# Performance work log

Measured on AMD Instinct MI355X. Metric: run time of the kernel, lower is better.

The kernel has to match this reference:

```python
import jax, jax.numpy as jnp
import numpy as np

N_NODES = 100000
N_EDGES = 1600000
IN_CH = 128
OUT_CH = 32
HID = 2 * OUT_CH


def setup_inputs() -> dict:
    key = jax.random.key(0)
    k1, k2, k3, k4 = jax.random.split(key, 4)
    x = jax.random.normal(k1, (N_NODES, IN_CH), dtype=jnp.float32)
    edge_index = jax.random.randint(k2, (2, N_EDGES), 0, N_NODES, dtype=jnp.int64)
    W1 = jax.random.normal(k3, (IN_CH, HID), dtype=jnp.float32) / np.sqrt(IN_CH)
    b1 = jnp.zeros((HID,), dtype=jnp.float32)
    W2 = jax.random.normal(k4, (HID, OUT_CH), dtype=jnp.float32) / np.sqrt(HID)
    b2 = jnp.zeros((OUT_CH,), dtype=jnp.float32)
    return {"x": x, "edge_index": edge_index, "W1": W1, "b1": b1, "W2": W2, "b2": b2}


def _gcn_norm(edge_index, n_nodes):
    # GCNConv default: add self-loops, symmetric deg^{-1/2} normalization.
    loop = jnp.arange(n_nodes, dtype=edge_index.dtype)
    src = jnp.concatenate([edge_index[0], loop])
    dst = jnp.concatenate([edge_index[1], loop])
    deg = jax.ops.segment_sum(jnp.ones_like(dst, dtype=jnp.float32), dst, num_segments=n_nodes)
    dinv = jnp.where(deg > 0, jax.lax.rsqrt(deg), 0.0)
    norm = dinv[src] * dinv[dst]  # [E + N]
    return src, dst, norm


def _gcn_conv(h, W, b, src, dst, norm, n_nodes):
    m = h @ W                      # transform first (small GEMM)
    msg = m[src] * norm[:, None]   # gather + scale per edge
    agg = jax.ops.segment_sum(msg, dst, num_segments=n_nodes)  # scatter-add
    return agg + b


def reference(x, edge_index, W1, b1, W2, b2):
    n = x.shape[0]
    src, dst, norm = _gcn_norm(edge_index, n)
    h = jax.nn.relu(_gcn_conv(x, W1, b1, src, dst, norm, n))
    return _gcn_conv(h, W2, b2, src, dst, norm, n)
```

## Files before the change

kernel.cpp:

```cpp
#include <hip/hip_runtime.h>

#define IN_CH 128
#define HID 64
#define OUT_CH 32
#define BUCKET_CAP 6144
#define NB_MAX 512

typedef _Float16 f16x8 __attribute__((ext_vector_type(8)));
typedef float f32x4 __attribute__((ext_vector_type(4)));

__device__ __forceinline__ unsigned short f32_to_bf16(float f) {
    union { float f; unsigned int u; } v; v.f = f;
    unsigned int u = v.u;
    u += 0x7FFFu + ((u >> 16) & 1u);
    return (unsigned short)(u >> 16);
}
__device__ __forceinline__ float bf16_to_f32(unsigned short h) {
    union { unsigned int u; float f; } v; v.u = ((unsigned int)h) << 16;
    return v.f;
}
__device__ __forceinline__ float bf16_lo(unsigned int u) {
    union { unsigned int u; float f; } v; v.u = u << 16; return v.f;
}
__device__ __forceinline__ float bf16_hi(unsigned int u) {
    union { unsigned int u; float f; } v; v.u = u & 0xFFFF0000u; return v.f;
}

__device__ __forceinline__ int load_idx(const void* e, long long i, int is64) {
    if (is64) return ((const int*)e)[2 * i];
    return ((const int*)e)[i];
}

__global__ __launch_bounds__(256) void binA_kernel(
    const void* __restrict__ edges, long long E,
    int* __restrict__ bucket_cur, unsigned int* __restrict__ entries, int nb) {
    __shared__ int hist[NB_MAX];
    __shared__ int cbase[NB_MAX];
    __shared__ int s_is64;
    const int tid = threadIdx.x;

    if (tid < 64) {
        int v = ((const int*)edges)[2 * tid + 1];
        unsigned long long nz = __ballot(v != 0);
        if (tid == 0) s_is64 = (nz == 0ull) ? 1 : 0;
    }
    for (int i = tid; i < nb; i += 256) hist[i] = 0;
    __syncthreads();
    const int is64 = s_is64;

    const long long per = (E + gridDim.x - 1) / gridDim.x;
    const long long lo = blockIdx.x * per;
    const long long hi = (lo + per < E) ? lo + per : E;

    for (long long i = lo + tid; i < hi; i += 256) {
        int dst = load_idx(edges, E + i, is64);
        atomicAdd(&hist[dst >> 8], 1);
    }
    __syncthreads();
    for (int i = tid; i < nb; i += 256) {
        int c = hist[i];
        int base = (c > 0) ? atomicAdd(&bucket_cur[i], c) : 0;
        cbase[i] = base;
        hist[i] = 0;
    }
    __syncthreads();
    for (long long i = lo + tid; i < hi; i += 256) {
        int src = load_idx(edges, i, is64);
        int dst = load_idx(edges, E + i, is64);
        int b = dst >> 8;
        int rel = cbase[b] + atomicAdd(&hist[b], 1);
        if (rel < BUCKET_CAP)
            entries[(long long)b * BUCKET_CAP + rel] = ((unsigned)src << 8) | (unsigned)(dst & 255);
    }
}

__global__ __launch_bounds__(256) void binB1_kernel(
    const unsigned int* __restrict__ entries, const int* __restrict__ bucket_cur,
    int* __restrict__ counts, int* __restrict__ row_off, float* __restrict__ dinv,
    int n) {
    __shared__ int hist[256];
    __shared__ int scan[256];
    const int b   = blockIdx.x;
    const int tid = threadIdx.x;
    const long long seg = (long long)b * BUCKET_CAP;
    int cnt = bucket_cur[b];
    if (cnt > BUCKET_CAP) cnt = BUCKET_CAP;

    hist[tid] = 0;
    __syncthreads();
    for (int i = tid; i < cnt; i += 256)
        atomicAdd(&hist[entries[seg + i] & 255], 1);
    __syncthreads();

    int v = hist[tid];
    scan[tid] = v;
    __syncthreads();
    for (int off = 1; off < 256; off <<= 1) {
        int t = (tid >= off) ? scan[tid - off] : 0;
        __syncthreads();
        scan[tid] += t;
        __syncthreads();
    }
    int ex = scan[tid] - v;
    int node = (b << 8) + tid;
    if (node < n) {
        counts[node]  = v;
        row_off[node] = (int)seg + ex;
        dinv[node]    = rsqrtf((float)v + 1.0f);
    }
}

__global__ __launch_bounds__(256) void binB2_kernel(
    const unsigned int* __restrict__ entries, const int* __restrict__ bucket_cur,
    const int* __restrict__ row_off, const float* __restrict__ dinv,
    int2* __restrict__ ew, int n) {
    __shared__ int cur[256];
    __shared__ float ldi[256];
    const int b   = blockIdx.x;
    const int tid = threadIdx.x;
    const long long seg = (long long)b * BUCKET_CAP;
    int cnt = bucket_cur[b];
    if (cnt > BUCKET_CAP) cnt = BUCKET_CAP;

    int node = (b << 8) + tid;
    cur[tid] = (node < n) ? row_off[node] - (int)seg : 0;
    ldi[tid] = (node < n) ? dinv[node] : 0.f;
    __syncthreads();

    for (int i = tid; i < cnt; i += 256) {
        unsigned e = entries[seg + i];
        int d = (int)(e & 255u);
        int s = (int)(e >> 8);
        int r = atomicAdd(&cur[d], 1);
        float w = dinv[s] * ldi[d];
        int2 o; o.x = s; o.y = __float_as_int(w);
        ew[seg + r] = o;
    }
}

__global__ __launch_bounds__(256) void gemm1_kernel(
    const float* __restrict__ x, const float* __restrict__ W1,
    unsigned short* __restrict__ m1bf, int n) {
    const int lane = threadIdx.x & 63;
    const int wid  = threadIdx.x >> 6;
    const int m    = lane & 15;
    const int g    = lane >> 4;
    const int Rw   = blockIdx.x * 64 + wid * 16;

    f16x8 wf[4][4];
#pragma unroll
    for (int t = 0; t < 4; ++t) {
        const float* wp = W1 + (t * 32 + g * 8) * HID + m;
#pragma unroll
        for (int c = 0; c < 4; ++c) {
#pragma unroll
            for (int j = 0; j < 8; ++j)
                wf[c][t][j] = (_Float16)wp[j * HID + c * 16];
        }
    }

    int rl = Rw + m;
    if (rl >= n) rl = n - 1;
    const float* xr = x + (long long)rl * IN_CH;

    f32x4 acc[4] = {};

#pragma unroll
    for (int t = 0; t < 4; ++t) {
        float4 xa = *(const float4*)(xr + t * 32 + g * 8);
        float4 xb = *(const float4*)(xr + t * 32 + g * 8 + 4);
        f16x8 af;
        af[0] = (_Float16)xa.x; af[1] = (_Float16)xa.y;
        af[2] = (_Float16)xa.z; af[3] = (_Float16)xa.w;
        af[4] = (_Float16)xb.x; af[5] = (_Float16)xb.y;
        af[6] = (_Float16)xb.z; af[7] = (_Float16)xb.w;
#pragma unroll
        for (int c = 0; c < 4; ++c)
            acc[c] = __builtin_amdgcn_mfma_f32_16x16x32_f16(af, wf[c][t], acc[c], 0, 0, 0);
    }

#pragma unroll
    for (int c = 0; c < 4; ++c) {
#pragma unroll
        for (int r = 0; r < 4; ++r) {
            int row = Rw + g * 4 + r;
            if (row < n)
                m1bf[(long long)row * HID + c * 16 + m] = f32_to_bf16(acc[c][r]);
        }
    }
}

#define PADH 132
__global__ __launch_bounds__(256) void gemm2_kernel(
    const unsigned short* __restrict__ hbf, const float* __restrict__ W2,
    unsigned short* __restrict__ m2bf, int n) {
    __shared__ __align__(16) float sW[HID * OUT_CH];
    __shared__ __align__(16) float sH[HID * PADH];
    const int tid = threadIdx.x;

    {
        const float4* Wv = (const float4*)W2;
        float4* sWv = (float4*)sW;
        for (int i = tid; i < HID * OUT_CH / 4; i += 256) sWv[i] = Wv[i];
    }

    const int R0 = blockIdx.x * 128;
    for (int i = tid; i < 128 * 8; i += 256) {
        int r = i >> 3;
        int q = i & 7;
        int row = R0 + r;
        uint4 v = make_uint4(0u, 0u, 0u, 0u);
        if (row < n)
            v = ((const uint4*)(hbf + (long long)row * HID))[q];
        int k0 = q * 8;
        sH[(k0 + 0) * PADH + r] = bf16_lo(v.x);
        sH[(k0 + 1) * PADH + r] = bf16_hi(v.x);
        sH[(k0 + 2) * PADH + r] = bf16_lo(v.y);
        sH[(k0 + 3) * PADH + r] = bf16_hi(v.y);
        sH[(k0 + 4) * PADH + r] = bf16_lo(v.z);
        sH[(k0 + 5) * PADH + r] = bf16_hi(v.z);
        sH[(k0 + 6) * PADH + r] = bf16_lo(v.w);
        sH[(k0 + 7) * PADH + r] = bf16_hi(v.w);
    }
    __syncthreads();

    const int tx = tid & 7;
    const int ty = tid >> 3;
    float acc[4][4] = {};
    const float* pH = sH + ty * 4;
    const float* pW = sW + tx * 4;
#pragma unroll 8
    for (int k = 0; k < HID; ++k) {
        float4 hv = *(const float4*)(pH + k * PADH);
        float4 wv = *(const float4*)(pW + k * OUT_CH);
        acc[0][0] += hv.x * wv.x; acc[0][1] += hv.x * wv.y;
        acc[0][2] += hv.x * wv.z; acc[0][3] += hv.x * wv.w;
        acc[1][0] += hv.y * wv.x; acc[1][1] += hv.y * wv.y;
        acc[1][2] += hv.y * wv.z; acc[1][3] += hv.y * wv.w;
        acc[2][0] += hv.z * wv.x; acc[2][1] += hv.z * wv.y;
        acc[2][2] += hv.z * wv.z; acc[2][3] += hv.z * wv.w;
        acc[3][0] += hv.w * wv.x; acc[3][1] += hv.w * wv.y;
        acc[3][2] += hv.w * wv.z; acc[3][3] += hv.w * wv.w;
    }

#pragma unroll
    for (int i = 0; i < 4; ++i) {
        int row = R0 + ty * 4 + i;
        if (row < n) {
            ushort4 o;
            o.x = f32_to_bf16(acc[i][0]);
            o.y = f32_to_bf16(acc[i][1]);
            o.z = f32_to_bf16(acc[i][2]);
            o.w = f32_to_bf16(acc[i][3]);
            *(ushort4*)(m2bf + (long long)row * OUT_CH + tx * 4) = o;
        }
    }
}

__global__ __launch_bounds__(256) void gather64_kernel(
    const int* __restrict__ row_off, const int* __restrict__ counts,
    const int2* __restrict__ ew, const float* __restrict__ dinv,
    const unsigned short* __restrict__ m1bf, const float* __restrict__ b1,
    unsigned short* __restrict__ hbf, int n) {
    const int node = blockIdx.x * 8 + (threadIdx.x >> 5);
    const int l    = threadIdx.x & 31;
    if (node >= n) return;
    const int start = row_off[node];
    const int cnt   = counts[node];

    float a0 = 0.f, a1 = 0.f;
    int j = 0;
    for (; j + 15 < cnt; j += 16) {
        int2 e[16];
#pragma unroll
        for (int u = 0; u < 16; ++u) e[u] = ew[start + j + u];
        unsigned v[16];
#pragma unroll
        for (int u = 0; u < 16; ++u)
            v[u] = *(const unsigned*)(m1bf + (unsigned)(e[u].x * HID) + l * 2);
#pragma unroll
        for (int u = 0; u < 16; ++u) {
            float w = __int_as_float(e[u].y);
            a0 += bf16_lo(v[u]) * w;
            a1 += bf16_hi(v[u]) * w;
        }
    }
    for (; j + 7 < cnt; j += 8) {
        int2 e[8];
#pragma unroll
        for (int u = 0; u < 8; ++u) e[u] = ew[start + j + u];
        unsigned v[8];
#pragma unroll
        for (int u = 0; u < 8; ++u)
            v[u] = *(const unsigned*)(m1bf + (unsigned)(e[u].x * HID) + l * 2);
#pragma unroll
        for (int u = 0; u < 8; ++u) {
            float w = __int_as_float(e[u].y);
            a0 += bf16_lo(v[u]) * w;
            a1 += bf16_hi(v[u]) * w;
        }
    }
    for (; j + 3 < cnt; j += 4) {
        int2 e[4];
#pragma unroll
        for (int u = 0; u < 4; ++u) e[u] = ew[start + j + u];
        unsigned v[4];
#pragma unroll
        for (int u = 0; u < 4; ++u)
            v[u] = *(const unsigned*)(m1bf + (unsigned)(e[u].x * HID) + l * 2);
#pragma unroll
        for (int u = 0; u < 4; ++u) {
            float w = __int_as_float(e[u].y);
            a0 += bf16_lo(v[u]) * w;
            a1 += bf16_hi(v[u]) * w;
        }
    }
    for (; j < cnt; ++j) {
        int2 e = ew[start + j];
        unsigned v = *(const unsigned*)(m1bf + (unsigned)(e.x * HID) + l * 2);
        float w = __int_as_float(e.y);
        a0 += bf16_lo(v) * w;
        a1 += bf16_hi(v) * w;
    }

    float dd = dinv[node];
    float ss = dd * dd;
    unsigned sv = *(const unsigned*)(m1bf + (unsigned)(node * HID) + l * 2);
    ushort2 o;
    o.x = f32_to_bf16(fmaxf(a0 + bf16_lo(sv) * ss + b1[l * 2],     0.f));
    o.y = f32_to_bf16(fmaxf(a1 + bf16_hi(sv) * ss + b1[l * 2 + 1], 0.f));
    *(ushort2*)(hbf + (unsigned)(node * HID) + l * 2) = o;
}

__global__ __launch_bounds__(256) void gather32_kernel(
    const int* __restrict__ row_off, const int* __restrict__ counts,
    const int2* __restrict__ ew, const float* __restrict__ dinv,
    const unsigned short* __restrict__ m2bf, const float* __restrict__ b2,
    float* __restrict__ out, int n) {
    const int node = blockIdx.x * 8 + (threadIdx.x >> 5);
    const int l    = threadIdx.x & 31;
    if (node >= n) return;
    const int start = row_off[node];
    const int cnt   = counts[node];

    float acc = 0.f;
    int j = 0;
    for (; j + 15 < cnt; j += 16) {
        int2 e[16];
#pragma unroll
        for (int u = 0; u < 16; ++u) e[u] = ew[start + j + u];
        unsigned short v[16];
#pragma unroll
        for (int u = 0; u < 16; ++u)
            v[u] = m2bf[(unsigned)(e[u].x * OUT_CH) + l];
#pragma unroll
        for (int u = 0; u < 16; ++u)
            acc += bf16_to_f32(v[u]) * __int_as_float(e[u].y);
    }
    for (; j + 7 < cnt; j += 8) {
        int2 e[8];
#pragma unroll
        for (int u = 0; u < 8; ++u) e[u] = ew[start + j + u];
        unsigned short v[8];
#pragma unroll
        for (int u = 0; u < 8; ++u)
            v[u] = m2bf[(unsigned)(e[u].x * OUT_CH) + l];
#pragma unroll
        for (int u = 0; u < 8; ++u)
            acc += bf16_to_f32(v[u]) * __int_as_float(e[u].y);
    }
    for (; j + 3 < cnt; j += 4) {
        int2 e[4];
#pragma unroll
        for (int u = 0; u < 4; ++u) e[u] = ew[start + j + u];
        unsigned short v[4];
#pragma unroll
        for (int u = 0; u < 4; ++u)
            v[u] = m2bf[(unsigned)(e[u].x * OUT_CH) + l];
#pragma unroll
        for (int u = 0; u < 4; ++u)
            acc += bf16_to_f32(v[u]) * __int_as_float(e[u].y);
    }
    for (; j < cnt; ++j) {
        int2 e = ew[start + j];
        acc += bf16_to_f32(m2bf[(unsigned)(e.x * OUT_CH) + l]) * __int_as_float(e.y);
    }

    float dd = dinv[node];
    float self = bf16_to_f32(m2bf[(unsigned)(node * OUT_CH) + l]);
    out[(unsigned)(node * OUT_CH) + l] = acc + self * dd * dd + b2[l];
}

extern "C" void kernel_launch(void* const* d_in, const int* in_sizes, int n_in,
                              void* d_out, int out_size, void* d_ws, size_t ws_size,
                              hipStream_t stream) {
    const float* x     = (const float*)d_in[0];
    const void*  edges = d_in[1];
    const float* W1    = (const float*)d_in[2];
    const float* b1    = (const float*)d_in[3];
    const float* W2    = (const float*)d_in[4];
    const float* b2    = (const float*)d_in[5];
    float* out = (float*)d_out;

    const int n = in_sizes[0] / IN_CH;
    const long long E = (long long)in_sizes[1] / 2;
    const int nb = (n + 255) / 256;

    float* ws         = (float*)d_ws;
    float* dinv       = ws;
    unsigned short* m1bf = (unsigned short*)(ws + n);
    unsigned short* m2bf = m1bf;
    float* agg        = ws + n + (long long)n * HID / 2;
    unsigned int* entries = (unsigned int*)agg;
    unsigned short* hbf   = (unsigned short*)agg;
    int*   counts     = (int*)(agg + (long long)n * HID);
    int*   row_off    = counts + n;
    int*   bucket_cur = row_off + n;
    int2*  ew         = (int2*)(bucket_cur + NB_MAX);

    hipMemsetAsync(bucket_cur, 0, NB_MAX * sizeof(int), stream);

    binA_kernel<<<256, 256, 0, stream>>>(edges, E, bucket_cur, entries, nb);
    binB1_kernel<<<nb, 256, 0, stream>>>(entries, bucket_cur, counts, row_off, dinv, n);
    binB2_kernel<<<nb, 256, 0, stream>>>(entries, bucket_cur, row_off, dinv, ew, n);

    gemm1_kernel<<<(n + 63) / 64, 256, 0, stream>>>(x, W1, m1bf, n);
    gather64_kernel<<<(n + 7) / 8, 256, 0, stream>>>(
        row_off, counts, ew, dinv, m1bf, b1, hbf, n);

    gemm2_kernel<<<(n + 127) / 128, 256, 0, stream>>>(hbf, W2, m2bf, n);
    gather32_kernel<<<(n + 7) / 8, 256, 0, stream>>>(
        row_off, counts, ew, dinv, m2bf, b2, out, n);
}
```

Baseline: 257.5 us.

## Fold symmetric norm into GEMM outputs and channel-slice feature layout for gathers

The per-edge weight is dropped: dinv[src] is folded into the GEMM outputs and dinv[dst] is applied once per node, so the edge list stores only source indices (4 bytes instead of 8). Node features are stored in channel-block slices of 8 or 4 channels, and the gather kernels process one slice per block. This is meant to shrink each slice's footprint so it stays cache-resident during the random gathers. Edge indices are read with nontemporal loads. The cost is that every slice re-reads the full edge list (8x index traffic), each lane gathers only 2 bytes per edge, and the workspace no longer aliases buffers, so it grows.

```diff
diff --git a/kernel.cpp b/kernel.cpp
--- a/kernel.cpp
+++ b/kernel.cpp
@@ -24,6 +24,9 @@
 }
 __device__ __forceinline__ float bf16_hi(unsigned int u) {
     union { unsigned int u; float f; } v; v.u = u & 0xFFFF0000u; return v.f;
+}
+__device__ __forceinline__ int nt_load(const int* p) {
+    return __builtin_nontemporal_load(p);
 }
 
 __device__ __forceinline__ int load_idx(const void* e, long long i, int is64) {
@@ -112,10 +115,8 @@
 
 __global__ __launch_bounds__(256) void binB2_kernel(
     const unsigned int* __restrict__ entries, const int* __restrict__ bucket_cur,
-    const int* __restrict__ row_off, const float* __restrict__ dinv,
-    int2* __restrict__ ew, int n) {
+    const int* __restrict__ row_off, int* __restrict__ es, int n) {
     __shared__ int cur[256];
-    __shared__ float ldi[256];
     const int b   = blockIdx.x;
     const int tid = threadIdx.x;
     const long long seg = (long long)b * BUCKET_CAP;
@@ -124,7 +125,6 @@
 
     int node = (b << 8) + tid;
     cur[tid] = (node < n) ? row_off[node] - (int)seg : 0;
-    ldi[tid] = (node < n) ? dinv[node] : 0.f;
     __syncthreads();
 
     for (int i = tid; i < cnt; i += 256) {
@@ -132,15 +132,13 @@
         int d = (int)(e & 255u);
         int s = (int)(e >> 8);
         int r = atomicAdd(&cur[d], 1);
-        float w = dinv[s] * ldi[d];
-        int2 o; o.x = s; o.y = __float_as_int(w);
-        ew[seg + r] = o;
+        es[seg + r] = s;
     }
 }
 
 __global__ __launch_bounds__(256) void gemm1_kernel(
     const float* __restrict__ x, const float* __restrict__ W1,
-    unsigned short* __restrict__ m1bf, int n) {
+    const float* __restrict__ dinv, unsigned short* __restrict__ m1s, int n) {
     const int lane = threadIdx.x & 63;
     const int wid  = threadIdx.x >> 6;
     const int m    = lane & 15;
@@ -180,20 +178,80 @@
     }
 
 #pragma unroll
-    for (int c = 0; c < 4; ++c) {
-#pragma unroll
-        for (int r = 0; r < 4; ++r) {
-            int row = Rw + g * 4 + r;
-            if (row < n)
-                m1bf[(long long)row * HID + c * 16 + m] = f32_to_bf16(acc[c][r]);
+    for (int r = 0; r < 4; ++r) {
+        int row = Rw + g * 4 + r;
+        if (row < n) {
+            float dd = dinv[row];
+#pragma unroll
+            for (int c = 0; c < 4; ++c) {
+                int ch = c * 16 + m;
+                m1s[((size_t)(ch >> 3) * n + row) * 8 + (ch & 7)] =
+                    f32_to_bf16(acc[c][r] * dd);
+            }
         }
     }
+}
+
+__global__ __launch_bounds__(256) void gather64_kernel(
+    const int* __restrict__ row_off, const int* __restrict__ counts,
+    const int* __restrict__ es, const float* __restrict__ dinv,
+    const unsigned short* __restrict__ m1s, const float* __restrict__ b1,
+    unsigned short* __restrict__ hs, int n) {
+    const int cblk = blockIdx.x & 7;
+    const int node = (blockIdx.x >> 3) * 32 + (threadIdx.x >> 3);
+    const int l    = threadIdx.x & 7;
+    if (node >= n) return;
+    const int start = row_off[node];
+    const int cnt   = counts[node];
+    const unsigned short* slice = m1s + (size_t)cblk * n * 8;
+
+    float acc = 0.f;
+    int j = 0;
+    for (; j + 15 < cnt; j += 16) {
+        int s[16];
+#pragma unroll
+        for (int u = 0; u < 16; ++u) s[u] = nt_load(es + start + j + u);
+        unsigned short v[16];
+#pragma unroll
+        for (int u = 0; u < 16; ++u) v[u] = slice[(unsigned)s[u] * 8 + l];
+#pragma unroll
+        for (int u = 0; u < 16; ++u) acc += bf16_to_f32(v[u]);
+    }
+    for (; j + 7 < cnt; j += 8) {
+        int s[8];
+#pragma unroll
+        for (int u = 0; u < 8; ++u) s[u] = nt_load(es + start + j + u);
+        unsigned short v[8];
+#pragma unroll
+        for (int u = 0; u < 8; ++u) v[u] = slice[(unsigned)s[u] * 8 + l];
+#pragma unroll
+        for (int u = 0; u < 8; ++u) acc += bf16_to_f32(v[u]);
+    }
+    for (; j + 3 < cnt; j += 4) {
+        int s[4];
+#pragma unroll
+        for (int u = 0; u < 4; ++u) s[u] = nt_load(es + start + j + u);
+        unsigned short v[4];
+#pragma unroll
+        for (int u = 0; u < 4; ++u) v[u] = slice[(unsigned)s[u] * 8 + l];
+#pragma unroll
+        for (int u = 0; u < 4; ++u) acc += bf16_to_f32(v[u]);
+    }
+    for (; j < cnt; ++j) {
+        int s = nt_load(es + start + j);
+        acc += bf16_to_f32(slice[(unsigned)s * 8 + l]);
+    }
+
+    float dd   = dinv[node];
+    float self = bf16_to_f32(slice[(unsigned)node * 8 + l]);
+    float o = (acc + self) * dd + b1[cblk * 8 + l];
+    hs[((size_t)cblk * n + node) * 8 + l] = f32_to_bf16(fmaxf(o, 0.f));
 }
 
 #define PADH 132
 __global__ __launch_bounds__(256) void gemm2_kernel(
-    const unsigned short* __restrict__ hbf, const float* __restrict__ W2,
-    unsigned short* __restrict__ m2bf, int n) {
+    const unsigned short* __restrict__ hs, const float* __restrict__ W2,
+    const float* __restrict__ dinv, unsigned short* __restrict__ m2s, int n) {
     __shared__ __align__(16) float sW[HID * OUT_CH];
     __shared__ __align__(16) float sH[HID * PADH];
     const int tid = threadIdx.x;
@@ -206,12 +264,12 @@
 
     const int R0 = blockIdx.x * 128;
     for (int i = tid; i < 128 * 8; i += 256) {
-        int r = i >> 3;
-        int q = i & 7;
+        int q = i >> 7;
+        int r = i & 127;
         int row = R0 + r;
         uint4 v = make_uint4(0u, 0u, 0u, 0u);
         if (row < n)
-            v = ((const uint4*)(hbf + (long long)row * HID))[q];
+            v = *(const uint4*)(hs + ((size_t)q * n + row) * 8);
         int k0 = q * 8;
         sH[(k0 + 0) * PADH + r] = bf16_lo(v.x);
         sH[(k0 + 1) * PADH + r] = bf16_hi(v.x);
@@ -247,148 +305,70 @@
     for (int i = 0; i < 4; ++i) {
         int row = R0 + ty * 4 + i;
         if (row < n) {
+            float dd = dinv[row];
             ushort4 o;
-            o.x = f32_to_bf16(acc[i][0]);
-            o.y = f32_to_bf16(acc[i][1]);
-            o.z = f32_to_bf16(acc[i][2]);
-            o.w = f32_to_bf16(acc[i][3]);
-            *(ushort4*)(m2bf + (long long)row * OUT_CH + tx * 4) = o;
+            o.x = f32_to_bf16(acc[i][0] * dd);
+            o.y = f32_to_bf16(acc[i][1] * dd);
+            o.z = f32_to_bf16(acc[i][2] * dd);
+            o.w = f32_to_bf16(acc[i][3] * dd);
+            *(ushort4*)(m2s + ((size_t)tx * n + row) * 4) = o;
         }
     }
 }
 
-__global__ __launch_bounds__(256) void gather64_kernel(
+__global__ __launch_bounds__(256) void gather32_kernel(
     const int* __restrict__ row_off, const int* __restrict__ counts,
-    const int2* __restrict__ ew, const float* __restrict__ dinv,
-    const unsigned short* __restrict__ m1bf, const float* __restrict__ b1,
-    unsigned short* __restrict__ hbf, int n) {
-    const int node = blockIdx.x * 8 + (threadIdx.x >> 5);
-    const int l    = threadIdx.x & 31;
+    const int* __restrict__ es, const float* __restrict__ dinv,
+    const unsigned short* __restrict__ m2s, const float* __restrict__ b2,
+    float* __restrict__ out, int n) {
+    const int cblk = blockIdx.x & 7;
+    const int node = (blockIdx.x >> 3) * 64 + (threadIdx.x >> 2);
+    const int l    = threadIdx.x & 3;
     if (node >= n) return;
     const int start = row_off[node];
     const int cnt   = counts[node];
-
-    float a0 = 0.f, a1 = 0.f;
-    int j = 0;
-    for (; j + 15 < cnt; j += 16) {
-        int2 e[16];
-#pragma unroll
-        for (int u = 0; u < 16; ++u) e[u] = ew[start + j + u];
-        unsigned v[16];
-#pragma unroll
-        for (int u = 0; u < 16; ++u)
-            v[u] = *(const unsigned*)(m1bf + (unsigned)(e[u].x * HID) + l * 2);
-#pragma unroll
-        for (int u = 0; u < 16; ++u) {
-            float w = __int_as_float(e[u].y);
-            a0 += bf16_lo(v[u]) * w;
-            a1 += bf16_hi(v[u]) * w;
-        }
-    }
-    for (; j + 7 < cnt; j += 8) {
-        int2 e[8];
-#pragma unroll
-        for (int u = 0; u < 8; ++u) e[u] = ew[start + j + u];
-        unsigned v[8];
-#pragma unroll
-        for (int u = 0; u < 8; ++u)
-            v[u] = *(const unsigned*)(m1bf + (unsigned)(e[u].x * HID) + l * 2);
-#pragma unroll
-        for (int u = 0; u < 8; ++u) {
-            float w = __int_as_float(e[u].y);
-            a0 += bf16_lo(v[u]) * w;
-            a1 += bf16_hi(v[u]) * w;
-        }
-    }
-    for (; j + 3 < cnt; j += 4) {
-        int2 e[4];
-#pragma unroll
-        for (int u = 0; u < 4; ++u) e[u] = ew[start + j + u];
-        unsigned v[4];
-#pragma unroll
-        for (int u = 0; u < 4; ++u)
-            v[u] = *(const unsigned*)(m1bf + (unsigned)(e[u].x * HID) + l * 2);
-#pragma unroll
-        for (int u = 0; u < 4; ++u) {
-            float w = __int_as_float(e[u].y);
-            a0 += bf16_lo(v[u]) * w;
-            a1 += bf16_hi(v[u]) * w;
-        }
-    }
-    for (; j < cnt; ++j) {
-        int2 e = ew[start + j];
-        unsigned v = *(const unsigned*)(m1bf + (unsigned)(e.x * HID) + l * 2);
-        float w = __int_as_float(e.y);
-        a0 += bf16_lo(v) * w;
-        a1 += bf16_hi(v) * w;
-    }
-
-    float dd = dinv[node];
-    float ss = dd * dd;
-    unsigned sv = *(const unsigned*)(m1bf + (unsigned)(node * HID) + l * 2);
-    ushort2 o;
-    o.x = f32_to_bf16(fmaxf(a0 + bf16_lo(sv) * ss + b1[l * 2],     0.f));
-    o.y = f32_to_bf16(fmaxf(a1 + bf16_hi(sv) * ss + b1[l * 2 + 1], 0.f));
-    *(ushort2*)(hbf + (unsigned)(node * HID) + l * 2) = o;
-}
-
-__global__ __launch_bounds__(256) void gather32_kernel(
-    const int* __restrict__ row_off, const int* __restrict__ counts,
-    const int2* __restrict__ ew, const float* __restrict__ dinv,
-    const unsigned short* __restrict__ m2bf, const float* __restrict__ b2,
-    float* __restrict__ out, int n) {
-    const int node = blockIdx.x * 8 + (threadIdx.x >> 5);
-    const int l    = threadIdx.x & 31;
-    if (node >= n) return;
-    const int start = row_off[node];
-    const int cnt   = counts[node];
+    const unsigned short* slice = m2s + (size_t)cblk * n * 4;
 
     float acc = 0.f;
     int j = 0;
     for (; j + 15 < cnt; j += 16) {
-        int2 e[16];
-#pragma unroll
-        for (int u = 0; u < 16; ++u) e[u] = ew[start + j + u];
+        int s[16];
+#pragma unroll
+        for (int u = 0; u < 16; ++u) s[u] = nt_load(es + start + j + u);
         unsigned short v[16];
 #pragma unroll
-        for (int u = 0; u < 16; ++u)
-            v[u] = m2bf[(unsigned)(e[u].x * OUT_CH) + l];
-#pragma unroll
-        for (int u = 0; u < 16; ++u)
-            acc += bf16_to_f32(v[u]) * __int_as_float(e[u].y);
+        for (int u = 0; u < 16; ++u) v[u] = slice[(unsigned)s[u] * 4 + l];
+#pragma unroll
+        for (int u = 0; u < 16; ++u) acc += bf16_to_f32(v[u]);
     }
     for (; j + 7 < cnt; j += 8) {
-        int2 e[8];
-#pragma unroll
-        for (int u = 0; u < 8; ++u) e[u] = ew[start + j + u];
+        int s[8];
+#pragma unroll
+        for (int u = 0; u < 8; ++u) s[u] = nt_load(es + start + j + u);
         unsigned short v[8];
 #pragma unroll
-        for (int u = 0; u < 8; ++u)
-            v[u] = m2bf[(unsigned)(e[u].x * OUT_CH) + l];
-#pragma unroll
-        for (int u = 0; u < 8; ++u)
-            acc += bf16_to_f32(v[u]) * __int_as_float(e[u].y);
+        for (int u = 0; u < 8; ++u) v[u] = slice[(unsigned)s[u] * 4 + l];
+#pragma unroll
+        for (int u = 0; u < 8; ++u) acc += bf16_to_f32(v[u]);
     }
     for (; j + 3 < cnt; j += 4) {
-        int2 e[4];
-#pragma unroll
-        for (int u = 0; u < 4; ++u) e[u] = ew[start + j + u];
+        int s[4];
+#pragma unroll
+        for (int u = 0; u < 4; ++u) s[u] = nt_load(es + start + j + u);
         unsigned short v[4];
 #pragma unroll
-        for (int u = 0; u < 4; ++u)
-            v[u] = m2bf[(unsigned)(e[u].x * OUT_CH) + l];
-#pragma unroll
-        for (int u = 0; u < 4; ++u)
-            acc += bf16_to_f32(v[u]) * __int_as_float(e[u].y);
+        for (int u = 0; u < 4; ++u) v[u] = slice[(unsigned)s[u] * 4 + l];
+#pragma unroll
+        for (int u = 0; u < 4; ++u) acc += bf16_to_f32(v[u]);
     }
     for (; j < cnt; ++j) {
-        int2 e = ew[start + j];
-        acc += bf16_to_f32(m2bf[(unsigned)(e.x * OUT_CH) + l]) * __int_as_float(e.y);
-    }
-
-    float dd = dinv[node];
-    float self = bf16_to_f32(m2bf[(unsigned)(node * OUT_CH) + l]);
-    out[(unsigned)(node * OUT_CH) + l] = acc + self * dd * dd + b2[l];
+        int s = nt_load(es + start + j);
+        acc += bf16_to_f32(slice[(unsigned)s * 4 + l]);
+    }
+
+    float dd   = dinv[node];
+    float self = bf16_to_f32(slice[(unsigned)node * 4 + l]);
+    out[(size_t)node * OUT_CH + cblk * 4 + l] = (acc + self) * dd + b2[cblk * 4 + l];
 }
 
 extern "C" void kernel_launch(void* const* d_in, const int* in_sizes, int n_in,
@@ -405,30 +385,30 @@
     const int n = in_sizes[0] / IN_CH;
     const long long E = (long long)in_sizes[1] / 2;
     const int nb = (n + 255) / 256;
-
-    float* ws         = (float*)d_ws;
-    float* dinv       = ws;
-    unsigned short* m1bf = (unsigned short*)(ws + n);
-    unsigned short* m2bf = m1bf;
-    float* agg        = ws + n + (long long)n * HID / 2;
-    unsigned int* entries = (unsigned int*)agg;
-    unsigned short* hbf   = (unsigned short*)agg;
-    int*   counts     = (int*)(agg + (long long)n * HID);
-    int*   row_off    = counts + n;
-    int*   bucket_cur = row_off + n;
-    int2*  ew         = (int2*)(bucket_cur + NB_MAX);
+    const size_t cap = (size_t)nb * BUCKET_CAP;
+
+    float* ws            = (float*)d_ws;
+    float* dinv          = ws;
+    int*   counts        = (int*)(ws + n);
+    int*   row_off       = counts + n;
+    int*   bucket_cur    = row_off + n;
+    unsigned int* entries = (unsigned int*)(bucket_cur + NB_MAX);
+    int*   es            = (int*)(entries + cap);
+    unsigned short* m1s  = (unsigned short*)(es + cap);
+    unsigned short* hs   = m1s + (size_t)n * HID;
+    unsigned short* m2s  = hs + (size_t)n * HID;
 
     hipMemsetAsync(bucket_cur, 0, NB_MAX * sizeof(int), stream);
 
     binA_kernel<<<256, 256, 0, stream>>>(edges, E, bucket_cur, entries, nb);
     binB1_kernel<<<nb, 256, 0, stream>>>(entries, bucket_cur, counts, row_off, dinv, n);
-    binB2_kernel<<<nb, 256, 0, stream>>>(entries, bucket_cur, row_off, dinv, ew, n);
-
-    gemm1_kernel<<<(n + 63) / 64, 256, 0, stream>>>(x, W1, m1bf, n);
-    gather64_kernel<<<(n + 7) / 8, 256, 0, stream>>>(
-        row_off, counts, ew, dinv, m1bf, b1, hbf, n);
-
-    gemm2_kernel<<<(n + 127) / 128, 256, 0, stream>>>(hbf, W2, m2bf, n);
-    gather32_kernel<<<(n + 7) / 8, 256, 0, stream>>>(
-        row_off, counts, ew, dinv, m2bf, b2, out, n);
-}
+    binB2_kernel<<<nb, 256, 0, stream>>>(entries, bucket_cur, row_off, es, n);
+
+    gemm1_kernel<<<(n + 63) / 64, 256, 0, stream>>>(x, W1, dinv, m1s, n);
+    gather64_kernel<<<((n + 31) / 32) * 8, 256, 0, stream>>>(
+        row_off, counts, es, dinv, m1s, b1, hs, n);
+
+    gemm2_kernel<<<(n + 127) / 128, 256, 0, stream>>>(hs, W2, dinv, m2s, n);
+    gather32_kernel<<<((n + 63) / 64) * 8, 256, 0, stream>>>(
+        row_off, counts, es, dinv, m2s, b2, out, n);
+}
```

Result: slower. 448.2 us (+74.0%).
